# Kernel optimization log

Measured on AMD Instinct MI355X. Metric: run time of the kernel, lower is better.

The kernel has to match this reference:

```python
import jax, jax.numpy as jnp
import numpy as np

B, S, H = 4, 4096, 2880
E, K = 32, 4


def setup_inputs() -> dict:
    key = jax.random.key(0)
    k1, k2 = jax.random.split(key)
    hidden_states = jax.random.normal(k1, (B, S, H), dtype=jnp.float32)
    # router weight, scaled like a typical init (std ~ 1/sqrt(H))
    weight = jax.random.normal(k2, (E, H), dtype=jnp.float32) / np.sqrt(H)
    bias = jnp.zeros((E,), dtype=jnp.float32)
    return {"hidden_states": hidden_states, "weight": weight, "bias": bias}


def reference(hidden_states, weight, bias):
    b, s, h = hidden_states.shape
    x = hidden_states.reshape(-1, h)                     # [T, H]
    logits = jnp.einsum('th,eh->te', x, weight) + bias   # [T, E]
    # select top-k logits (sorted descending), then softmax over the subset
    topk_logits, topk_idx = jax.lax.top_k(logits, K)     # [T, K]
    topk_weight = jax.nn.softmax(topk_logits.astype(jnp.float32), axis=-1)
    return topk_idx, topk_weight
```

## Files before the change

### kernel.cpp

```cpp
#include <hip/hip_runtime.h>
#include <math.h>

#define H_DIM 2880
#define E_NUM 32
#define TOPK 4
#define TT 64
#define KW 96
#define NSTG 30
#define GRP 772
#define XB 0
#define XBS 6176
#define WB 12352
#define WBS 3088
#define REDR 36
#define LGTO 18432
#define SMSZ 20736

#define GLD16(gp, lp)                                                  \
    __builtin_amdgcn_global_load_lds(                                  \
        (const __attribute__((address_space(1))) void*)(gp),           \
        (__attribute__((address_space(3))) void*)(lp), 16, 0, 0)

__global__ __launch_bounds__(512, 2) void gate_fused(
    const float* __restrict__ x, const float* __restrict__ w,
    const float* __restrict__ bias, float* __restrict__ out, int T) {
    __shared__ float sm[SMSZ];
    const int tid = threadIdx.x;
    const int lane = tid & 63;
    const int wq = __builtin_amdgcn_readfirstlane(tid >> 6);
    const int tg = lane & 7;
    const int eg = (lane >> 3) & 3;
    const int kg = lane >> 5;
    const int t0 = blockIdx.x * TT;

    const float* gx[3]; const float* gw[3]; int lx[3], lw[3];
#pragma unroll
    for (int i = 0; i < 3; ++i) {
        const int d = i * 256 + lane * 4;
        const int r = d / KW, kk = d % KW;
        gx[i] = x + (size_t)(t0 + wq * 8 + r) * H_DIM + kk;
        lx[i] = XB + wq * GRP + d;
        gw[i] = w + (size_t)((wq & 3) * 8 + r) * H_DIM + kk;
        lw[i] = WB + (wq & 3) * GRP + d;
    }

    float acc[64];
#pragma unroll
    for (int i = 0; i < 64; ++i) acc[i] = 0.f;

#pragma unroll
    for (int i = 0; i < 3; ++i) GLD16(gx[i], &sm[lx[i]]);
    if (wq < 4) {
#pragma unroll
        for (int i = 0; i < 3; ++i) GLD16(gw[i], &sm[lw[i]]);
    }

    const int koA = wq * 12 + kg * 4;
    const int koB = wq * 12 + 8 + kg * 2;

    for (int s = 0; s < NSTG; ++s) {
        __syncthreads();
        if (s + 1 < NSTG) {
            const size_t go = (size_t)(s + 1) * KW;
            const int pb = (s + 1) & 1;
#pragma unroll
            for (int i = 0; i < 3; ++i) GLD16(gx[i] + go, &sm[lx[i] + pb * XBS]);
            if (wq < 4) {
#pragma unroll
                for (int i = 0; i < 3; ++i) GLD16(gw[i] + go, &sm[lw[i] + pb * WBS]);
            }
        }
        const int p = s & 1;
        const float* xbp = &sm[XB + p * XBS + tg * GRP];
        const float* wbp = &sm[WB + p * WBS + eg * GRP];

        float4 xa[8], wa[8];
#pragma unroll
        for (int i = 0; i < 8; ++i) xa[i] = *(const float4*)(xbp + i * KW + koA);
#pragma unroll
        for (int j = 0; j < 8; ++j) wa[j] = *(const float4*)(wbp + j * KW + koA);
#pragma unroll
        for (int i = 0; i < 8; ++i)
#pragma unroll
            for (int j = 0; j < 8; ++j)
                acc[i * 8 + j] += xa[i].x * wa[j].x + xa[i].y * wa[j].y +
                                  xa[i].z * wa[j].z + xa[i].w * wa[j].w;

        float2 x2[8], w2[8];
#pragma unroll
        for (int i = 0; i < 8; ++i) x2[i] = *(const float2*)(xbp + i * KW + koB);
#pragma unroll
        for (int j = 0; j < 8; ++j) w2[j] = *(const float2*)(wbp + j * KW + koB);
#pragma unroll
        for (int i = 0; i < 8; ++i)
#pragma unroll
            for (int j = 0; j < 8; ++j)
                acc[i * 8 + j] += x2[i].x * w2[j].x + x2[i].y * w2[j].y;
    }

    __syncthreads();

#pragma unroll
    for (int d = 0; d < 64; ++d) acc[d] += __shfl_xor(acc[d], 32, 64);

    if (kg == 0) {
#pragma unroll
        for (int i = 0; i < 8; ++i) {
            float* rp = &sm[wq * 2304 + (tg * 8 + i) * REDR + eg * 8];
            *(float4*)(rp + 0) = make_float4(acc[i * 8 + 0], acc[i * 8 + 1],
                                             acc[i * 8 + 2], acc[i * 8 + 3]);
            *(float4*)(rp + 4) = make_float4(acc[i * 8 + 4], acc[i * 8 + 5],
                                             acc[i * 8 + 6], acc[i * 8 + 7]);
        }
    }
    __syncthreads();

    {
        const int tok = tid >> 3, e4 = (tid & 7) * 4;
        float4 sg = *(const float4*)(bias + e4);
#pragma unroll
        for (int q = 0; q < 8; ++q) {
            float4 v = *(const float4*)&sm[q * 2304 + tok * REDR + e4];
            sg.x += v.x; sg.y += v.y; sg.z += v.z; sg.w += v.w;
        }
        *(float4*)&sm[LGTO + tok * REDR + e4] = sg;
    }
    __syncthreads();

    if (tid < 64) {
        const int t = t0 + tid;
        float logit[E_NUM];
#pragma unroll
        for (int j = 0; j < 8; ++j) {
            float4 v = *(const float4*)&sm[LGTO + tid * REDR + j * 4];
            logit[j * 4] = v.x; logit[j * 4 + 1] = v.y;
            logit[j * 4 + 2] = v.z; logit[j * 4 + 3] = v.w;
        }

        int idx[TOPK];
        float val[TOPK];
#pragma unroll
        for (int k = 0; k < TOPK; ++k) {
            float best = -INFINITY;
            int bi = 0;
#pragma unroll
            for (int e = 0; e < E_NUM; ++e) {
                bool taken = false;
                for (int p = 0; p < k; ++p) taken = taken || (idx[p] == e);
                float v = logit[e];
                if (!taken && v > best) { best = v; bi = e; }
            }
            idx[k] = bi;
            val[k] = best;
        }
        float ex[TOPK], ssum = 0.f;
#pragma unroll
        for (int k = 0; k < TOPK; ++k) { ex[k] = expf(val[k] - val[0]); ssum += ex[k]; }
        const float inv = 1.f / ssum;

        *(float4*)(out + (size_t)t * 4) =
            make_float4((float)idx[0], (float)idx[1], (float)idx[2], (float)idx[3]);
        *(float4*)(out + (size_t)T * 4 + (size_t)t * 4) =
            make_float4(ex[0] * inv, ex[1] * inv, ex[2] * inv, ex[3] * inv);
    }
}

extern "C" void kernel_launch(void* const* d_in, const int* in_sizes, int n_in,
                              void* d_out, int out_size, void* d_ws, size_t ws_size,
                              hipStream_t stream) {
    const float* x    = (const float*)d_in[0];
    const float* w    = (const float*)d_in[1];
    const float* bias = (const float*)d_in[2];
    float* out = (float*)d_out;

    const int T = in_sizes[0] / H_DIM;

    gate_fused<<<dim3(T / TT), 512, 0, stream>>>(x, w, bias, out, T);
}
```

Baseline: 285.8 us.

## Halve token tile to 32 with 256-thread blocks and 16-way K split

Shrinks each block from 64 to 32 tokens and from 8 to 4 waves, remapping lanes so each thread covers a 4x4 token/expert group with a 16-way K split reduced by two shuffles. All four waves now load weights, and shared memory per block drops. This doubles the grid to spread work across more CUs and raise occupancy. In exchange the router weight tile is reloaded twice as often across blocks and the in-register reduction gets longer.

```diff
diff --git a/kernel.cpp b/kernel.cpp
--- a/kernel.cpp
+++ b/kernel.cpp
@@ -4,33 +4,33 @@
 #define H_DIM 2880
 #define E_NUM 32
 #define TOPK 4
-#define TT 64
+#define TT 32
 #define KW 96
 #define NSTG 30
 #define GRP 772
 #define XB 0
-#define XBS 6176
-#define WB 12352
+#define XBS 3088
+#define WB 6176
 #define WBS 3088
+#define SMSZ 12352
 #define REDR 36
-#define LGTO 18432
-#define SMSZ 20736
+#define LGTO 4608
 
 #define GLD16(gp, lp)                                                  \
     __builtin_amdgcn_global_load_lds(                                  \
         (const __attribute__((address_space(1))) void*)(gp),           \
         (__attribute__((address_space(3))) void*)(lp), 16, 0, 0)
 
-__global__ __launch_bounds__(512, 2) void gate_fused(
+__global__ __launch_bounds__(256, 2) void gate_fused(
     const float* __restrict__ x, const float* __restrict__ w,
     const float* __restrict__ bias, float* __restrict__ out, int T) {
     __shared__ float sm[SMSZ];
     const int tid = threadIdx.x;
     const int lane = tid & 63;
     const int wq = __builtin_amdgcn_readfirstlane(tid >> 6);
-    const int tg = lane & 7;
-    const int eg = (lane >> 3) & 3;
-    const int kg = lane >> 5;
+    const int tt = lane & 3;
+    const int et = (lane >> 2) & 3;
+    const int ksl = lane >> 4;
     const int t0 = blockIdx.x * TT;
 
     const float* gx[3]; const float* gw[3]; int lx[3], lw[3];
@@ -39,9 +39,9 @@
         const int d = i * 256 + lane * 4;
         const int r = d / KW, kk = d % KW;
         gx[i] = x + (size_t)(t0 + wq * 8 + r) * H_DIM + kk;
+        gw[i] = w + (size_t)(wq * 8 + r) * H_DIM + kk;
         lx[i] = XB + wq * GRP + d;
-        gw[i] = w + (size_t)((wq & 3) * 8 + r) * H_DIM + kk;
-        lw[i] = WB + (wq & 3) * GRP + d;
+        lw[i] = WB + wq * GRP + d;
     }
 
     float acc[64];
@@ -50,13 +50,12 @@
 
 #pragma unroll
     for (int i = 0; i < 3; ++i) GLD16(gx[i], &sm[lx[i]]);
-    if (wq < 4) {
 #pragma unroll
-        for (int i = 0; i < 3; ++i) GLD16(gw[i], &sm[lw[i]]);
-    }
+    for (int i = 0; i < 3; ++i) GLD16(gw[i], &sm[lw[i]]);
 
-    const int koA = wq * 12 + kg * 4;
-    const int koB = wq * 12 + 8 + kg * 2;
+    const int ks = wq * 4 + ksl;
+    const int koA = ks * 4;
+    const int koB = 64 + ks * 2;
 
     for (int s = 0; s < NSTG; ++s) {
         __syncthreads();
@@ -65,14 +64,12 @@
             const int pb = (s + 1) & 1;
 #pragma unroll
             for (int i = 0; i < 3; ++i) GLD16(gx[i] + go, &sm[lx[i] + pb * XBS]);
-            if (wq < 4) {
 #pragma unroll
-                for (int i = 0; i < 3; ++i) GLD16(gw[i] + go, &sm[lw[i] + pb * WBS]);
-            }
+            for (int i = 0; i < 3; ++i) GLD16(gw[i] + go, &sm[lw[i] + pb * WBS]);
         }
         const int p = s & 1;
-        const float* xbp = &sm[XB + p * XBS + tg * GRP];
-        const float* wbp = &sm[WB + p * WBS + eg * GRP];
+        const float* xbp = &sm[XB + p * XBS + tt * GRP];
+        const float* wbp = &sm[WB + p * WBS + et * GRP];
 
         float4 xa[8], wa[8];
 #pragma unroll
@@ -101,12 +98,15 @@
     __syncthreads();
 
 #pragma unroll
-    for (int d = 0; d < 64; ++d) acc[d] += __shfl_xor(acc[d], 32, 64);
+    for (int d = 0; d < 64; ++d) {
+        acc[d] += __shfl_xor(acc[d], 16, 64);
+        acc[d] += __shfl_xor(acc[d], 32, 64);
+    }
 
-    if (kg == 0) {
+    if (ksl == 0) {
 #pragma unroll
         for (int i = 0; i < 8; ++i) {
-            float* rp = &sm[wq * 2304 + (tg * 8 + i) * REDR + eg * 8];
+            float* rp = &sm[wq * (TT * REDR) + (tt * 8 + i) * REDR + et * 8];
             *(float4*)(rp + 0) = make_float4(acc[i * 8 + 0], acc[i * 8 + 1],
                                              acc[i * 8 + 2], acc[i * 8 + 3]);
             *(float4*)(rp + 4) = make_float4(acc[i * 8 + 4], acc[i * 8 + 5],
@@ -119,15 +119,15 @@
         const int tok = tid >> 3, e4 = (tid & 7) * 4;
         float4 sg = *(const float4*)(bias + e4);
 #pragma unroll
-        for (int q = 0; q < 8; ++q) {
-            float4 v = *(const float4*)&sm[q * 2304 + tok * REDR + e4];
+        for (int q = 0; q < 4; ++q) {
+            float4 v = *(const float4*)&sm[q * (TT * REDR) + tok * REDR + e4];
             sg.x += v.x; sg.y += v.y; sg.z += v.z; sg.w += v.w;
         }
         *(float4*)&sm[LGTO + tok * REDR + e4] = sg;
     }
     __syncthreads();
 
-    if (tid < 64) {
+    if (tid < TT) {
         const int t = t0 + tid;
         float logit[E_NUM];
 #pragma unroll
@@ -175,5 +175,5 @@
 
     const int T = in_sizes[0] / H_DIM;
 
-    gate_fused<<<dim3(T / TT), 512, 0, stream>>>(x, w, bias, out, T);
+    gate_fused<<<dim3(T / TT), 256, 0, stream>>>(x, w, bias, out, T);
 }
```

Measured after the change: 275.9 us. 3.5% less time.
